# Kernel optimization log

Hardware: AMD Instinct MI355X
Metric: run time of the kernel (lower is better)

Reference implementation:

```python
import jax, jax.numpy as jnp
import numpy as np

HEADS = 8

def _ln(x, g, b):
    m = jnp.mean(x, -1, keepdims=True)
    v = jnp.var(x, -1, keepdims=True)
    return (x - m) * jax.lax.rsqrt(v + 1e-5) * g + b

def _mha(q, kv, W, b, key_valid):
    # W: [4,E,E] (q,k,v,out proj), b: [4,E]; key_valid: [Sk] bool mask over kv positions
    B, Sq, E = q.shape
    Sk = kv.shape[1]
    D = E // HEADS
    qh = (q @ W[0] + b[0]).reshape(B, Sq, HEADS, D)
    kh = (kv @ W[1] + b[1]).reshape(B, Sk, HEADS, D)
    vh = (kv @ W[2] + b[2]).reshape(B, Sk, HEADS, D)
    s = jnp.einsum('bqhd,bkhd->bhqk', qh, kh) / jnp.sqrt(jnp.asarray(D, q.dtype))
    s = jnp.where(key_valid[None, None, None, :], s, jnp.asarray(-1e9, q.dtype))
    o = jnp.einsum('bhqk,bkhd->bqhd', jax.nn.softmax(s, -1), vh).reshape(B, Sq, E)
    return o @ W[3] + b[3]

def _posenc(S, E):
    pos = np.arange(S)[:, None].astype(np.float32)
    i = np.arange(0, E, 2).astype(np.float32)[None, :]
    ang = pos / np.power(10000.0, i / E)
    pe = np.zeros((S, E), np.float32)
    pe[:, 0::2] = np.sin(ang)
    pe[:, 1::2] = np.cos(ang)
    return jnp.asarray(pe)

def _forward(noise, seeds, inemb_W, inemb_b, g_attn_W, g_attn_b, g_cross_W, g_cross_b,
             g_ffn_W1, g_ffn_b1, g_ffn_W2, g_ffn_b2, g_ln_g, g_ln_b,
             o_attn_W, o_attn_b, o_ffn_W1, o_ffn_b1, o_ffn_W2, o_ffn_b2, o_ln_g, o_ln_b,
             w2v, soft_W, soft_b):
    B, S, E = noise.shape
    V = soft_W.shape[1]
    # inEmb: M stacked linear layers (no activation)
    w = noise
    for i in range(inemb_W.shape[0]):
        w = w @ inemb_W[i] + inemb_b[i]
    pe = _posenc(S, E)[None]  # [1,S,E]
    nB = g_attn_W.shape[0]
    nO = o_attn_W.shape[0]

    def step(carry, t):
        Ybuf, out_sent = carry
        valid = jnp.arange(S) <= t  # grown-sequence mask (no KV cache in original)
        x = Ybuf + pe
        for i in range(nB):  # generator: outTrans decoder blocks (self + cross-attn to w)
            x = _ln(x + _mha(x, x, g_attn_W[i], g_attn_b[i], valid), g_ln_g[i, 0], g_ln_b[i, 0])
            x = _ln(x + _mha(x, w, g_cross_W[i], g_cross_b[i], valid), g_ln_g[i, 1], g_ln_b[i, 1])
            f = jax.nn.relu(x @ g_ffn_W1[i] + g_ffn_b1[i]) @ g_ffn_W2[i] + g_ffn_b2[i]
            x = _ln(x + f, g_ln_g[i, 2], g_ln_b[i, 2])
        for j in range(nO):  # outEmb: inTrans encoder blocks
            x = _ln(x + _mha(x, x, o_attn_W[j], o_attn_b[j], valid), o_ln_g[j, 0], o_ln_b[j, 0])
            f = jax.nn.relu(x @ o_ffn_W1[j] + o_ffn_b1[j]) @ o_ffn_W2[j] + o_ffn_b2[j]
            x = _ln(x + f, o_ln_g[j, 1], o_ln_b[j, 1])
        tok = x[:, t]  # [B,E]
        probs = jax.nn.softmax(tok @ soft_W + soft_b, axis=-1)  # [B,V]
        out_sent = jax.lax.dynamic_update_slice(out_sent, probs[:, None, :], (0, t, 0))
        emb = w2v[jnp.argmax(probs, axis=-1)]  # Word2Vec(one_hot(argmax)) == row lookup
        Ybuf = jax.lax.dynamic_update_slice(Ybuf, emb[:, None, :], (0, t, 0))
        return (Ybuf, out_sent), None

    init = (seeds, jnp.zeros((B, S, V), noise.dtype))
    (_, out_sent), _ = jax.lax.scan(step, init, jnp.arange(S))
    return out_sent

def setup_inputs():
    key = jax.random.key(0)
    ks = jax.random.split(key, 12)
    B, S, E, H, V = 32, 32, 512, 2048, 30000
    M, NB, NO = 2, 2, 1
    def rn(k, shape, s=0.02):
        return jax.random.normal(k, shape, jnp.float32) * s
    return {
        'noise': jax.random.normal(ks[0], (B, S, E), jnp.float32),
        'seeds': jax.random.normal(ks[1], (B, S, E), jnp.float32),
        'inemb_W': rn(ks[2], (M, E, E)), 'inemb_b': jnp.zeros((M, E), jnp.float32),
        'g_attn_W': rn(ks[3], (NB, 4, E, E)), 'g_attn_b': jnp.zeros((NB, 4, E), jnp.float32),
        'g_cross_W': rn(ks[4], (NB, 4, E, E)), 'g_cross_b': jnp.zeros((NB, 4, E), jnp.float32),
        'g_ffn_W1': rn(ks[5], (NB, E, H)), 'g_ffn_b1': jnp.zeros((NB, H), jnp.float32),
        'g_ffn_W2': rn(ks[6], (NB, H, E)), 'g_ffn_b2': jnp.zeros((NB, E), jnp.float32),
        'g_ln_g': jnp.ones((NB, 3, E), jnp.float32), 'g_ln_b': jnp.zeros((NB, 3, E), jnp.float32),
        'o_attn_W': rn(ks[7], (NO, 4, E, E)), 'o_attn_b': jnp.zeros((NO, 4, E), jnp.float32),
        'o_ffn_W1': rn(ks[8], (NO, E, H)), 'o_ffn_b1': jnp.zeros((NO, H), jnp.float32),
        'o_ffn_W2': rn(ks[9], (NO, H, E)), 'o_ffn_b2': jnp.zeros((NO, E), jnp.float32),
        'o_ln_g': jnp.ones((NO, 2, E), jnp.float32), 'o_ln_b': jnp.zeros((NO, 2, E), jnp.float32),
        'w2v': rn(ks[10], (V, E)),
        'soft_W': rn(ks[11], (E, V)), 'soft_b': jnp.zeros((V,), jnp.float32),
    }

def reference(noise, seeds, inemb_W, inemb_b, g_attn_W, g_attn_b, g_cross_W, g_cross_b,
              g_ffn_W1, g_ffn_b1, g_ffn_W2, g_ffn_b2, g_ln_g, g_ln_b,
              o_attn_W, o_attn_b, o_ffn_W1, o_ffn_b1, o_ffn_W2, o_ffn_b2, o_ln_g, o_ln_b,
              w2v, soft_W, soft_b):
    return _forward(noise, seeds, inemb_W, inemb_b, g_attn_W, g_attn_b, g_cross_W, g_cross_b,
                    g_ffn_W1, g_ffn_b1, g_ffn_W2, g_ffn_b2, g_ln_g, g_ln_b,
                    o_attn_W, o_attn_b, o_ffn_W1, o_ffn_b1, o_ffn_W2, o_ffn_b2, o_ln_g, o_ln_b,
                    w2v, soft_W, soft_b)
```

## Files before the change

### kernel.cpp

```cpp
#include <hip/hip_runtime.h>
#include <math.h>

#define E 512
#define S_MAX 32
#define BATCH 32
#define HEADS 8
#define DH 64
#define HID 2048
#define VOCAB 30000

__global__ void pe_kernel(float* __restrict__ PEp) {
    int s = blockIdx.x;
    for (int e = threadIdx.x; e < E; e += 256) {
        float expo = (float)(e & ~1) / (float)E;
        float den = powf(10000.0f, expo);
        float ang = (float)s / den;
        PEp[s * E + e] = (e & 1) ? cosf(ang) : sinf(ang);
    }
}

__global__ void build_x_kernel(float* __restrict__ X, const float* __restrict__ Ybuf,
                               const float* __restrict__ PEp, int Seff) {
    long idx = (long)blockIdx.x * 256 + threadIdx.x;
    long total = (long)BATCH * Seff * E;
    if (idx >= total) return;
    int e = (int)(idx & (E - 1));
    long m = idx >> 9;
    int b = (int)(m / Seff);
    int s = (int)(m - (long)b * Seff);
    X[idx] = Ybuf[((long)b * S_MAX + s) * E + e] + PEp[s * E + e];
}

template <int RELU>
__global__ __launch_bounds__(256) void gemm_kernel(const float* __restrict__ A,
                                                   const float* __restrict__ W,
                                                   const float* __restrict__ bias,
                                                   float* __restrict__ C,
                                                   int M, int N, int K,
                                                   long wz, long cz, long bz) {
    int z = blockIdx.z;
    W += (long)z * wz;
    C += (long)z * cz;
    bias += (long)z * bz;
    int n0 = blockIdx.x * 64;
    int m0 = blockIdx.y * 64;
    int tid = threadIdx.x;
    int tx = tid & 15, ty = tid >> 4;

    __shared__ float As[16][68];
    __shared__ float Ws[16][64];

    float acc[4][4];
#pragma unroll
    for (int i = 0; i < 4; i++)
#pragma unroll
        for (int j = 0; j < 4; j++) acc[i][j] = 0.f;

    for (int k0 = 0; k0 < K; k0 += 16) {
#pragma unroll
        for (int l = 0; l < 4; l++) {
            int idx = tid + l * 256;
            int m = idx >> 4, k = idx & 15;
            int mm = m0 + m;
            if (mm >= M) mm = M - 1;
            As[k][m] = A[(long)mm * K + k0 + k];
        }
#pragma unroll
        for (int l = 0; l < 4; l++) {
            int idx = tid + l * 256;
            int k = idx >> 6, n = idx & 63;
            Ws[k][n] = W[(long)(k0 + k) * N + n0 + n];
        }
        __syncthreads();
#pragma unroll
        for (int k = 0; k < 16; k++) {
            float a0 = As[k][ty * 4 + 0], a1 = As[k][ty * 4 + 1];
            float a2 = As[k][ty * 4 + 2], a3 = As[k][ty * 4 + 3];
            float w0 = Ws[k][tx * 4 + 0], w1 = Ws[k][tx * 4 + 1];
            float w2 = Ws[k][tx * 4 + 2], w3 = Ws[k][tx * 4 + 3];
            acc[0][0] += a0 * w0; acc[0][1] += a0 * w1; acc[0][2] += a0 * w2; acc[0][3] += a0 * w3;
            acc[1][0] += a1 * w0; acc[1][1] += a1 * w1; acc[1][2] += a1 * w2; acc[1][3] += a1 * w3;
            acc[2][0] += a2 * w0; acc[2][1] += a2 * w1; acc[2][2] += a2 * w2; acc[2][3] += a2 * w3;
            acc[3][0] += a3 * w0; acc[3][1] += a3 * w1; acc[3][2] += a3 * w2; acc[3][3] += a3 * w3;
        }
        __syncthreads();
    }
#pragma unroll
    for (int i = 0; i < 4; i++) {
        int m = m0 + ty * 4 + i;
        if (m < M) {
#pragma unroll
            for (int j = 0; j < 4; j++) {
                int n = n0 + tx * 4 + j;
                float v = acc[i][j] + bias[n];
                if (RELU) v = fmaxf(v, 0.f);
                C[(long)m * N + n] = v;
            }
        }
    }
}

__global__ __launch_bounds__(64) void attn_kernel(const float* __restrict__ Q,
                                                  const float* __restrict__ Kp,
                                                  const float* __restrict__ Vp,
                                                  float* __restrict__ O,
                                                  int Seff, int kvBatchStride) {
    int s = blockIdx.x, h = blockIdx.y, b = blockIdx.z;
    int lane = threadIdx.x;
    __shared__ float qs[DH];
    qs[lane] = Q[((long)(b * Seff + s)) * E + h * DH + lane];
    __syncthreads();

    float sc = -INFINITY;
    if (lane < Seff) {
        const float4* k4 = (const float4*)(Kp + (long)b * kvBatchStride + (long)lane * E + h * DH);
        const float4* q4 = (const float4*)qs;
        float acc = 0.f;
#pragma unroll
        for (int d = 0; d < DH / 4; d++) {
            float4 kv = k4[d];
            float4 qv = q4[d];
            acc += qv.x * kv.x;
            acc += qv.y * kv.y;
            acc += qv.z * kv.z;
            acc += qv.w * kv.w;
        }
        sc = acc * 0.125f;
    }
    float m = sc;
#pragma unroll
    for (int off = 32; off; off >>= 1) m = fmaxf(m, __shfl_xor(m, off));
    float p = (lane < Seff) ? expf(sc - m) : 0.f;
    float sum = p;
#pragma unroll
    for (int off = 32; off; off >>= 1) sum += __shfl_xor(sum, off);
    p = p / sum;

    float acc = 0.f;
    const float* vbase = Vp + (long)b * kvBatchStride + h * DH + lane;
    for (int k = 0; k < Seff; k++) {
        float pk = __shfl(p, k);
        acc = fmaf(pk, vbase[(long)k * E], acc);
    }
    O[((long)(b * Seff + s)) * E + h * DH + lane] = acc;
}

__global__ __launch_bounds__(64) void resid_ln_kernel(float* __restrict__ X,
                                                      const float* __restrict__ Dlt,
                                                      const float* __restrict__ g,
                                                      const float* __restrict__ bb) {
    long row = blockIdx.x;
    int lane = threadIdx.x;
    float* xr = X + row * E;
    const float* dr = Dlt + row * E;
    float v[8];
    float s = 0.f;
#pragma unroll
    for (int i = 0; i < 8; i++) {
        int e = lane + i * 64;
        v[i] = xr[e] + dr[e];
        s += v[i];
    }
#pragma unroll
    for (int off = 32; off; off >>= 1) s += __shfl_xor(s, off);
    float mean = s * (1.0f / E);
    float sq = 0.f;
#pragma unroll
    for (int i = 0; i < 8; i++) {
        float d = v[i] - mean;
        sq += d * d;
    }
#pragma unroll
    for (int off = 32; off; off >>= 1) sq += __shfl_xor(sq, off);
    float var = sq * (1.0f / E);
    float r = 1.0f / sqrtf(var + 1e-5f);
#pragma unroll
    for (int i = 0; i < 8; i++) {
        int e = lane + i * 64;
        xr[e] = (v[i] - mean) * r * g[e] + bb[e];
    }
}

__global__ __launch_bounds__(256) void logits_kernel(const float* __restrict__ X,
                                                     const float* __restrict__ SW,
                                                     const float* __restrict__ sb,
                                                     float* __restrict__ Lg,
                                                     int Seff, int t) {
    int nl = threadIdx.x & 63;
    int kq = threadIdx.x >> 6;
    int n = blockIdx.x * 64 + nl;
    bool nok = n < VOCAB;
    float acc[BATCH];
#pragma unroll
    for (int b = 0; b < BATCH; b++) acc[b] = 0.f;
    if (nok) {
        int k0 = kq * 128;
        for (int k = k0; k < k0 + 128; k++) {
            float wv = SW[(long)k * VOCAB + n];
#pragma unroll
            for (int b = 0; b < BATCH; b++) {
                acc[b] = fmaf(X[((long)(b * Seff + t)) * E + k], wv, acc[b]);
            }
        }
    }
    __shared__ float red[4][64];
    for (int b = 0; b < BATCH; b++) {
        red[kq][nl] = acc[b];
        __syncthreads();
        if (kq == 0 && nok) {
            float sum = red[0][nl] + red[1][nl] + red[2][nl] + red[3][nl] + sb[n];
            Lg[(long)b * VOCAB + n] = sum;
        }
        __syncthreads();
    }
}

__global__ __launch_bounds__(256) void softmax_out_kernel(const float* __restrict__ Lg,
                                                          float* __restrict__ Out,
                                                          const float* __restrict__ w2v,
                                                          float* __restrict__ Ybuf, int t) {
    int b = blockIdx.x;
    int tid = threadIdx.x;
    const float* lb = Lg + (long)b * VOCAB;
    __shared__ float red[256];

    float m = -INFINITY;
    for (int n = tid; n < VOCAB; n += 256) m = fmaxf(m, lb[n]);
    red[tid] = m;
    __syncthreads();
    for (int off = 128; off; off >>= 1) {
        if (tid < off) red[tid] = fmaxf(red[tid], red[tid + off]);
        __syncthreads();
    }
    m = red[0];
    __syncthreads();

    float s = 0.f;
    for (int n = tid; n < VOCAB; n += 256) s += expf(lb[n] - m);
    red[tid] = s;
    __syncthreads();
    for (int off = 128; off; off >>= 1) {
        if (tid < off) red[tid] += red[tid + off];
        __syncthreads();
    }
    s = red[0];
    __syncthreads();

    float bestv = -1.0f;
    int besti = VOCAB;
    float* ob = Out + ((long)b * S_MAX + t) * VOCAB;
    for (int n = tid; n < VOCAB; n += 256) {
        float p = expf(lb[n] - m) / s;
        ob[n] = p;
        if (p > bestv) { bestv = p; besti = n; }
    }
    __shared__ float rv[256];
    __shared__ int ri[256];
    rv[tid] = bestv;
    ri[tid] = besti;
    __syncthreads();
    for (int off = 128; off; off >>= 1) {
        if (tid < off) {
            float v2 = rv[tid + off];
            int i2 = ri[tid + off];
            if (v2 > rv[tid] || (v2 == rv[tid] && i2 < ri[tid])) { rv[tid] = v2; ri[tid] = i2; }
        }
        __syncthreads();
    }
    int idx = ri[0];
    float* yb = Ybuf + ((long)b * S_MAX + t) * E;
    for (int e = tid; e < E; e += 256) yb[e] = w2v[(long)idx * E + e];
}

extern "C" void kernel_launch(void* const* d_in, const int* in_sizes, int n_in,
                              void* d_out, int out_size, void* d_ws, size_t ws_size,
                              hipStream_t stream) {
    const float* noise    = (const float*)d_in[0];
    const float* seeds    = (const float*)d_in[1];
    const float* inemb_W  = (const float*)d_in[2];
    const float* inemb_b  = (const float*)d_in[3];
    const float* g_attn_W = (const float*)d_in[4];
    const float* g_attn_b = (const float*)d_in[5];
    const float* g_cross_W= (const float*)d_in[6];
    const float* g_cross_b= (const float*)d_in[7];
    const float* g_ffn_W1 = (const float*)d_in[8];
    const float* g_ffn_b1 = (const float*)d_in[9];
    const float* g_ffn_W2 = (const float*)d_in[10];
    const float* g_ffn_b2 = (const float*)d_in[11];
    const float* g_ln_g   = (const float*)d_in[12];
    const float* g_ln_b   = (const float*)d_in[13];
    const float* o_attn_W = (const float*)d_in[14];
    const float* o_attn_b = (const float*)d_in[15];
    const float* o_ffn_W1 = (const float*)d_in[16];
    const float* o_ffn_b1 = (const float*)d_in[17];
    const float* o_ffn_W2 = (const float*)d_in[18];
    const float* o_ffn_b2 = (const float*)d_in[19];
    const float* o_ln_g   = (const float*)d_in[20];
    const float* o_ln_b   = (const float*)d_in[21];
    const float* w2v      = (const float*)d_in[22];
    const float* soft_W   = (const float*)d_in[23];
    const float* soft_b   = (const float*)d_in[24];
    float* out = (float*)d_out;
    float* ws = (float*)d_ws;

    const long EE  = (long)E * E;
    const long BSE = (long)BATCH * S_MAX * E;

    float* PE   = ws;
    float* WEMB = PE + 16384;
    float* KWVW = WEMB + BSE;
    float* YBUF = KWVW + 4 * BSE;
    float* X    = YBUF + BSE;
    float* QKV  = X + BSE;
    float* AOUT = QKV + 3 * BSE;
    float* TMP  = AOUT + BSE;
    float* HB   = TMP + BSE;
    float* LG   = HB + (long)BATCH * S_MAX * HID;

    auto GEMM = [&](const float* A, const float* W, const float* bias, float* C,
                    int M, int N, int K, int Z, long wz, long cz, long bz, bool relu) {
        dim3 g(N / 64, (M + 63) / 64, Z);
        if (relu)
            gemm_kernel<1><<<g, dim3(256), 0, stream>>>(A, W, bias, C, M, N, K, wz, cz, bz);
        else
            gemm_kernel<0><<<g, dim3(256), 0, stream>>>(A, W, bias, C, M, N, K, wz, cz, bz);
    };

    pe_kernel<<<dim3(S_MAX), dim3(256), 0, stream>>>(PE);
    hipMemcpyAsync(YBUF, seeds, BSE * sizeof(float), hipMemcpyDeviceToDevice, stream);

    GEMM(noise, inemb_W, inemb_b, QKV, BATCH * S_MAX, E, E, 1, 0, 0, 0, false);
    GEMM(QKV, inemb_W + EE, inemb_b + E, WEMB, BATCH * S_MAX, E, E, 1, 0, 0, 0, false);

    for (int i = 0; i < 2; i++) {
        GEMM(WEMB, g_cross_W + i * 4 * EE + EE, g_cross_b + i * 4 * E + E,
             KWVW + i * 2 * BSE, BATCH * S_MAX, E, E, 2, EE, BSE, E, false);
    }

    for (int t = 0; t < S_MAX; t++) {
        int Seff = t + 1;
        int Mrows = BATCH * Seff;
        long ME = (long)Mrows * E;
        int total = Mrows * E;

        build_x_kernel<<<dim3((total + 255) / 256), dim3(256), 0, stream>>>(X, YBUF, PE, Seff);

        for (int i = 0; i < 2; i++) {
            const float* AW = g_attn_W + i * 4 * EE;
            const float* Ab = g_attn_b + i * 4 * E;
            GEMM(X, AW, Ab, QKV, Mrows, E, E, 3, EE, ME, E, false);
            attn_kernel<<<dim3(Seff, HEADS, BATCH), dim3(64), 0, stream>>>(
                QKV, QKV + ME, QKV + 2 * ME, AOUT, Seff, Seff * E);
            GEMM(AOUT, AW + 3 * EE, Ab + 3 * E, TMP, Mrows, E, E, 1, 0, 0, 0, false);
            resid_ln_kernel<<<dim3(Mrows), dim3(64), 0, stream>>>(
                X, TMP, g_ln_g + (i * 3 + 0) * E, g_ln_b + (i * 3 + 0) * E);
            const float* CW = g_cross_W + i * 4 * EE;
            const float* Cb = g_cross_b + i * 4 * E;
            GEMM(X, CW, Cb, QKV, Mrows, E, E, 1, 0, 0, 0, false);
            attn_kernel<<<dim3(Seff, HEADS, BATCH), dim3(64), 0, stream>>>(
                QKV, KWVW + i * 2 * BSE, KWVW + i * 2 * BSE + BSE, AOUT, Seff, S_MAX * E);
            GEMM(AOUT, CW + 3 * EE, Cb + 3 * E, TMP, Mrows, E, E, 1, 0, 0, 0, false);
            resid_ln_kernel<<<dim3(Mrows), dim3(64), 0, stream>>>(
                X, TMP, g_ln_g + (i * 3 + 1) * E, g_ln_b + (i * 3 + 1) * E);
            GEMM(X, g_ffn_W1 + i * (long)E * HID, g_ffn_b1 + i * HID, HB, Mrows, HID, E,
                 1, 0, 0, 0, true);
            GEMM(HB, g_ffn_W2 + i * (long)HID * E, g_ffn_b2 + i * E, TMP, Mrows, E, HID,
                 1, 0, 0, 0, false);
            resid_ln_kernel<<<dim3(Mrows), dim3(64), 0, stream>>>(
                X, TMP, g_ln_g + (i * 3 + 2) * E, g_ln_b + (i * 3 + 2) * E);
        }
        GEMM(X, o_attn_W, o_attn_b, QKV, Mrows, E, E, 3, EE, ME, E, false);
        attn_kernel<<<dim3(Seff, HEADS, BATCH), dim3(64), 0, stream>>>(
            QKV, QKV + ME, QKV + 2 * ME, AOUT, Seff, Seff * E);
        GEMM(AOUT, o_attn_W + 3 * EE, o_attn_b + 3 * E, TMP, Mrows, E, E, 1, 0, 0, 0, false);
        resid_ln_kernel<<<dim3(Mrows), dim3(64), 0, stream>>>(X, TMP, o_ln_g, o_ln_b);
        GEMM(X, o_ffn_W1, o_ffn_b1, HB, Mrows, HID, E, 1, 0, 0, 0, true);
        GEMM(HB, o_ffn_W2, o_ffn_b2, TMP, Mrows, E, HID, 1, 0, 0, 0, false);
        resid_ln_kernel<<<dim3(Mrows), dim3(64), 0, stream>>>(X, TMP, o_ln_g + E, o_ln_b + E);

        logits_kernel<<<dim3((VOCAB + 63) / 64), dim3(256), 0, stream>>>(X, soft_W, soft_b, LG, Seff, t);
        softmax_out_kernel<<<dim3(BATCH), dim3(256), 0, stream>>>(LG, out, w2v, YBUF, t);
    }
}
```

Baseline: 32.73 ms.

## Replace FP32 SIMT GEMMs with three-way bf16-split MFMA GEMMs

Replaces the scalar FP32 tiled GEMM with an MFMA bf16 GEMM. To keep near-FP32 accuracy, each operand is split into high, mid and low bf16 parts and six cross-product MFMAs are accumulated. Weights are pre-split and transposed once per call when workspace allows, otherwise per GEMM. Producer kernels (build_x, attention, layernorm, GEMM epilogues) now emit split activations directly. This trades six MFMA passes and extra split storage and traffic for matrix-core throughput in place of FP32 FMA loops.

```diff
diff --git a/kernel.cpp b/kernel.cpp
--- a/kernel.cpp
+++ b/kernel.cpp
@@ -9,6 +9,26 @@
 #define HID 2048
 #define VOCAB 30000
 
+typedef unsigned short u16;
+typedef __attribute__((ext_vector_type(8))) short short8;
+typedef __attribute__((ext_vector_type(4))) float f32x4;
+
+__device__ __forceinline__ u16 f2bf(float x) {
+    union { float f; unsigned u; } v; v.f = x;
+    unsigned r = v.u + 0x7fffu + ((v.u >> 16) & 1u);
+    return (u16)(r >> 16);
+}
+__device__ __forceinline__ float bf2f(u16 h) {
+    union { unsigned u; float f; } v; v.u = ((unsigned)h) << 16;
+    return v.f;
+}
+__device__ __forceinline__ void split3(float x, u16& h, u16& m, u16& l) {
+    h = f2bf(x); float hf = bf2f(h);
+    float r1 = x - hf;
+    m = f2bf(r1); float mf = bf2f(m);
+    l = f2bf(r1 - mf);
+}
+
 __global__ void pe_kernel(float* __restrict__ PEp) {
     int s = blockIdx.x;
     for (int e = threadIdx.x; e < E; e += 256) {
@@ -20,81 +40,155 @@
 }
 
 __global__ void build_x_kernel(float* __restrict__ X, const float* __restrict__ Ybuf,
-                               const float* __restrict__ PEp, int Seff) {
+                               const float* __restrict__ PEp, int Seff,
+                               u16* __restrict__ Xh, u16* __restrict__ Xm, u16* __restrict__ Xl) {
     long idx = (long)blockIdx.x * 256 + threadIdx.x;
     long total = (long)BATCH * Seff * E;
     if (idx >= total) return;
     int e = (int)(idx & (E - 1));
-    long m = idx >> 9;
-    int b = (int)(m / Seff);
-    int s = (int)(m - (long)b * Seff);
-    X[idx] = Ybuf[((long)b * S_MAX + s) * E + e] + PEp[s * E + e];
-}
-
-template <int RELU>
-__global__ __launch_bounds__(256) void gemm_kernel(const float* __restrict__ A,
-                                                   const float* __restrict__ W,
-                                                   const float* __restrict__ bias,
-                                                   float* __restrict__ C,
-                                                   int M, int N, int K,
-                                                   long wz, long cz, long bz) {
+    long mm = idx >> 9;
+    int b = (int)(mm / Seff);
+    int s = (int)(mm - (long)b * Seff);
+    float v = Ybuf[((long)b * S_MAX + s) * E + e] + PEp[s * E + e];
+    X[idx] = v;
+    u16 h, m, l; split3(v, h, m, l);
+    Xh[idx] = h; Xm[idx] = m; Xl[idx] = l;
+}
+
+__global__ void split_act_kernel(const float* __restrict__ in, long n,
+                                 u16* __restrict__ Ph, u16* __restrict__ Pm, u16* __restrict__ Pl) {
+    long i = ((long)blockIdx.x * 256 + threadIdx.x) * 4;
+    if (i >= n) return;
+    float4 v = *(const float4*)(in + i);
+    u16 h, m, l;
+    split3(v.x, h, m, l); Ph[i] = h; Pm[i] = m; Pl[i] = l;
+    split3(v.y, h, m, l); Ph[i+1] = h; Pm[i+1] = m; Pl[i+1] = l;
+    split3(v.z, h, m, l); Ph[i+2] = h; Pm[i+2] = m; Pl[i+2] = l;
+    split3(v.w, h, m, l); Ph[i+3] = h; Pm[i+3] = m; Pl[i+3] = l;
+}
+
+__global__ __launch_bounds__(256) void wsplit_kernel(const float* __restrict__ W,
+                                                     u16* __restrict__ Ph, u16* __restrict__ Pm,
+                                                     u16* __restrict__ Pl,
+                                                     int K, int N, long wzin, long wzout) {
     int z = blockIdx.z;
-    W += (long)z * wz;
+    W += (long)z * wzin; Ph += (long)z * wzout; Pm += (long)z * wzout; Pl += (long)z * wzout;
+    int n0 = blockIdx.x * 32, k0 = blockIdx.y * 32;
+    __shared__ float T[32][33];
+    int tid = threadIdx.x;
+    int kk = tid >> 3, nn = (tid & 7) * 4;
+    float4 v = *(const float4*)&W[(long)(k0 + kk) * N + n0 + nn];
+    T[kk][nn + 0] = v.x; T[kk][nn + 1] = v.y; T[kk][nn + 2] = v.z; T[kk][nn + 3] = v.w;
+    __syncthreads();
+    int n = tid >> 3, k4 = (tid & 7) * 4;
+    u16 h[4], m[4], l[4];
+#pragma unroll
+    for (int j = 0; j < 4; j++) split3(T[k4 + j][n], h[j], m[j], l[j]);
+    long o = (long)(n0 + n) * K + k0 + k4;
+    *(ushort4*)&Ph[o] = make_ushort4(h[0], h[1], h[2], h[3]);
+    *(ushort4*)&Pm[o] = make_ushort4(m[0], m[1], m[2], m[3]);
+    *(ushort4*)&Pl[o] = make_ushort4(l[0], l[1], l[2], l[3]);
+}
+
+template <int RELU, int WF32, int WSPLIT>
+__global__ __launch_bounds__(256) void gemm_mfma(
+    const u16* __restrict__ Ah, const u16* __restrict__ Am, const u16* __restrict__ Al,
+    const u16* __restrict__ Wh, const u16* __restrict__ Wm, const u16* __restrict__ Wl,
+    const float* __restrict__ bias,
+    float* __restrict__ C, u16* __restrict__ Ch, u16* __restrict__ Cm, u16* __restrict__ Cl,
+    int M, int N, int K, long wz, long cz, long bz) {
+    int z = blockIdx.z;
+    const u16* Ap[3] = {Ah, Am, Al};
+    const u16* Bp[3] = {Wh + (long)z * wz, Wm + (long)z * wz, Wl + (long)z * wz};
+    bias += (long)z * bz;
     C += (long)z * cz;
-    bias += (long)z * bz;
-    int n0 = blockIdx.x * 64;
-    int m0 = blockIdx.y * 64;
-    int tid = threadIdx.x;
-    int tx = tid & 15, ty = tid >> 4;
-
-    __shared__ float As[16][68];
-    __shared__ float Ws[16][64];
-
-    float acc[4][4];
-#pragma unroll
-    for (int i = 0; i < 4; i++)
-#pragma unroll
-        for (int j = 0; j < 4; j++) acc[i][j] = 0.f;
-
-    for (int k0 = 0; k0 < K; k0 += 16) {
-#pragma unroll
-        for (int l = 0; l < 4; l++) {
-            int idx = tid + l * 256;
-            int m = idx >> 4, k = idx & 15;
-            int mm = m0 + m;
-            if (mm >= M) mm = M - 1;
-            As[k][m] = A[(long)mm * K + k0 + k];
-        }
-#pragma unroll
-        for (int l = 0; l < 4; l++) {
-            int idx = tid + l * 256;
-            int k = idx >> 6, n = idx & 63;
-            Ws[k][n] = W[(long)(k0 + k) * N + n0 + n];
-        }
-        __syncthreads();
-#pragma unroll
-        for (int k = 0; k < 16; k++) {
-            float a0 = As[k][ty * 4 + 0], a1 = As[k][ty * 4 + 1];
-            float a2 = As[k][ty * 4 + 2], a3 = As[k][ty * 4 + 3];
-            float w0 = Ws[k][tx * 4 + 0], w1 = Ws[k][tx * 4 + 1];
-            float w2 = Ws[k][tx * 4 + 2], w3 = Ws[k][tx * 4 + 3];
-            acc[0][0] += a0 * w0; acc[0][1] += a0 * w1; acc[0][2] += a0 * w2; acc[0][3] += a0 * w3;
-            acc[1][0] += a1 * w0; acc[1][1] += a1 * w1; acc[1][2] += a1 * w2; acc[1][3] += a1 * w3;
-            acc[2][0] += a2 * w0; acc[2][1] += a2 * w1; acc[2][2] += a2 * w2; acc[2][3] += a2 * w3;
-            acc[3][0] += a3 * w0; acc[3][1] += a3 * w1; acc[3][2] += a3 * w2; acc[3][3] += a3 * w3;
-        }
-        __syncthreads();
-    }
-#pragma unroll
-    for (int i = 0; i < 4; i++) {
-        int m = m0 + ty * 4 + i;
-        if (m < M) {
+    Ch += (long)z * cz; Cm += (long)z * cz; Cl += (long)z * cz;
+
+    int n0 = blockIdx.x * 64, m0 = blockIdx.y * 64;
+    int tid = threadIdx.x, lane = tid & 63, wid = tid >> 6;
+    int wr = wid >> 1, wc = wid & 1;
+
+    __shared__ u16 As[3][2048];
+    __shared__ u16 Bs[3][2048];
+
+    int srow = (tid >> 6) * 16 + (tid & 15);
+    int scol = ((tid >> 4) & 3) * 8;
+    int arow = m0 + srow; if (arow >= M) arow = M - 1;
+    int brow = n0 + srow;
+    long abase = (long)arow * K + scol;
+    long bbase = (long)brow * K + scol;
+
+    uint4 ra[3], rb[3];
+#pragma unroll
+    for (int p = 0; p < 3; p++) {
+        ra[p] = *(const uint4*)(Ap[p] + abase);
+        rb[p] = *(const uint4*)(Bp[p] + bbase);
+    }
+
+    f32x4 acc[2][2];
+#pragma unroll
+    for (int mi = 0; mi < 2; mi++)
+#pragma unroll
+        for (int ni = 0; ni < 2; ni++) acc[mi][ni] = (f32x4){0.f, 0.f, 0.f, 0.f};
+
+    int fro = (lane >> 4) * 128 + (lane & 15) * 8;
+    const int PA[6] = {0, 0, 1, 1, 0, 2};
+    const int PB[6] = {0, 1, 0, 1, 2, 0};
+
+    for (int k0 = 0; k0 < K; k0 += 32) {
+#pragma unroll
+        for (int p = 0; p < 3; p++) {
+            *(uint4*)&As[p][tid * 8] = ra[p];
+            *(uint4*)&Bs[p][tid * 8] = rb[p];
+        }
+        __syncthreads();
+        if (k0 + 32 < K) {
+#pragma unroll
+            for (int p = 0; p < 3; p++) {
+                ra[p] = *(const uint4*)(Ap[p] + abase + k0 + 32);
+                rb[p] = *(const uint4*)(Bp[p] + bbase + k0 + 32);
+            }
+        }
+        short8 af[3][2], bf[3][2];
+#pragma unroll
+        for (int p = 0; p < 3; p++) {
+#pragma unroll
+            for (int q = 0; q < 2; q++) {
+                af[p][q] = *(const short8*)&As[p][(wr * 2 + q) * 512 + fro];
+                bf[p][q] = *(const short8*)&Bs[p][(wc * 2 + q) * 512 + fro];
+            }
+        }
+#pragma unroll
+        for (int u = 0; u < 6; u++) {
+#pragma unroll
+            for (int mi = 0; mi < 2; mi++)
+#pragma unroll
+                for (int ni = 0; ni < 2; ni++)
+                    acc[mi][ni] = __builtin_amdgcn_mfma_f32_16x16x32_bf16(
+                        af[PA[u]][mi], bf[PB[u]][ni], acc[mi][ni], 0, 0, 0);
+        }
+        __syncthreads();
+    }
+
+#pragma unroll
+    for (int mi = 0; mi < 2; mi++) {
+#pragma unroll
+        for (int ni = 0; ni < 2; ni++) {
+            int col = n0 + wc * 32 + ni * 16 + (lane & 15);
+            float bv = bias[col];
 #pragma unroll
             for (int j = 0; j < 4; j++) {
-                int n = n0 + tx * 4 + j;
-                float v = acc[i][j] + bias[n];
-                if (RELU) v = fmaxf(v, 0.f);
-                C[(long)m * N + n] = v;
+                int row = m0 + wr * 32 + mi * 16 + (lane >> 4) * 4 + j;
+                if (row < M) {
+                    float v = acc[mi][ni][j] + bv;
+                    if (RELU) v = fmaxf(v, 0.f);
+                    long idx = (long)row * N + col;
+                    if (WF32) C[idx] = v;
+                    if (WSPLIT) {
+                        u16 hh, mm, ll; split3(v, hh, mm, ll);
+                        Ch[idx] = hh; Cm[idx] = mm; Cl[idx] = ll;
+                    }
+                }
             }
         }
     }
@@ -103,7 +197,8 @@
 __global__ __launch_bounds__(64) void attn_kernel(const float* __restrict__ Q,
                                                   const float* __restrict__ Kp,
                                                   const float* __restrict__ Vp,
-                                                  float* __restrict__ O,
+                                                  u16* __restrict__ Oh, u16* __restrict__ Om,
+                                                  u16* __restrict__ Ol,
                                                   int Seff, int kvBatchStride) {
     int s = blockIdx.x, h = blockIdx.y, b = blockIdx.z;
     int lane = threadIdx.x;
@@ -120,10 +215,7 @@
         for (int d = 0; d < DH / 4; d++) {
             float4 kv = k4[d];
             float4 qv = q4[d];
-            acc += qv.x * kv.x;
-            acc += qv.y * kv.y;
-            acc += qv.z * kv.z;
-            acc += qv.w * kv.w;
+            acc += qv.x * kv.x; acc += qv.y * kv.y; acc += qv.z * kv.z; acc += qv.w * kv.w;
         }
         sc = acc * 0.125f;
     }
@@ -142,13 +234,17 @@
         float pk = __shfl(p, k);
         acc = fmaf(pk, vbase[(long)k * E], acc);
     }
-    O[((long)(b * Seff + s)) * E + h * DH + lane] = acc;
+    long o = ((long)(b * Seff + s)) * E + h * DH + lane;
+    u16 hh, mm, ll; split3(acc, hh, mm, ll);
+    Oh[o] = hh; Om[o] = mm; Ol[o] = ll;
 }
 
 __global__ __launch_bounds__(64) void resid_ln_kernel(float* __restrict__ X,
                                                       const float* __restrict__ Dlt,
                                                       const float* __restrict__ g,
-                                                      const float* __restrict__ bb) {
+                                                      const float* __restrict__ bb,
+                                                      u16* __restrict__ Xh, u16* __restrict__ Xm,
+                                                      u16* __restrict__ Xl) {
     long row = blockIdx.x;
     int lane = threadIdx.x;
     float* xr = X + row * E;
@@ -177,7 +273,11 @@
 #pragma unroll
     for (int i = 0; i < 8; i++) {
         int e = lane + i * 64;
-        xr[e] = (v[i] - mean) * r * g[e] + bb[e];
+        float o = (v[i] - mean) * r * g[e] + bb[e];
+        xr[e] = o;
+        u16 hh, mm, ll; split3(o, hh, mm, ll);
+        long idx = row * E + e;
+        Xh[idx] = hh; Xm[idx] = mm; Xl[idx] = ll;
     }
 }
 
@@ -304,37 +404,91 @@
     float* ws = (float*)d_ws;
 
     const long EE  = (long)E * E;
+    const long EH  = (long)E * HID;
     const long BSE = (long)BATCH * S_MAX * E;
-
-    float* PE   = ws;
-    float* WEMB = PE + 16384;
-    float* KWVW = WEMB + BSE;
-    float* YBUF = KWVW + 4 * BSE;
-    float* X    = YBUF + BSE;
-    float* QKV  = X + BSE;
-    float* AOUT = QKV + 3 * BSE;
-    float* TMP  = AOUT + BSE;
-    float* HB   = TMP + BSE;
-    float* LG   = HB + (long)BATCH * S_MAX * HID;
-
-    auto GEMM = [&](const float* A, const float* W, const float* bias, float* C,
-                    int M, int N, int K, int Z, long wz, long cz, long bz, bool relu) {
+    const long BSH = (long)BATCH * S_MAX * HID;
+    const long WTOT = 46 * EE;
+
+    long off = 0;
+    float* PE   = ws + off; off += 16384;
+    float* YBUF = ws + off; off += BSE;
+    float* X    = ws + off; off += BSE;
+    float* TMP  = ws + off; off += BSE;
+    float* QKV  = ws + off; off += 3 * BSE;
+    float* KWVW = ws + off; off += 4 * BSE;
+    float* LG   = ws + off; off += 960000;
+    u16* XsH = (u16*)(ws + off); off += 3 * BSE / 2;
+    u16* XsM = XsH + BSE; u16* XsL = XsM + BSE;
+    u16* AOH = (u16*)(ws + off); off += 3 * BSE / 2;
+    u16* AOM = AOH + BSE; u16* AOL = AOM + BSE;
+    u16* HBH = (u16*)(ws + off); off += 3 * BSH / 2;
+    u16* HBM2 = HBH + BSH; u16* HBL = HBM2 + BSH;
+    long baseWords = off;
+
+    bool full = ws_size >= (size_t)(baseWords + 3 * WTOT / 2) * 4;
+    long WT_ELEMS = full ? WTOT : 4 * EE;
+    u16* WT_H = (u16*)(ws + baseWords);
+    u16* WT_M = WT_H + WT_ELEMS;
+    u16* WT_L = WT_M + WT_ELEMS;
+
+    const long OFF_INEMB = 0;
+    const long OFF_GATTN = 2 * EE;
+    const long OFF_GCROSS = 10 * EE;
+    const long OFF_OATTN = 18 * EE;
+    const long OFF_GF1 = 22 * EE;
+    const long OFF_GF2 = 30 * EE;
+    const long OFF_OF1 = 38 * EE;
+    const long OFF_OF2 = 42 * EE;
+
+    auto WSPL = [&](const float* Wsrc, long offFull, int K, int N, int z) -> long {
+        if (full) return offFull;
+        wsplit_kernel<<<dim3(N / 32, K / 32, z), dim3(256), 0, stream>>>(
+            Wsrc, WT_H, WT_M, WT_L, K, N, (long)K * N, (long)K * N);
+        return 0;
+    };
+
+    auto GEMM = [&](const u16* Ah, const u16* Am, const u16* Al, long woff,
+                    const float* bias, float* C, u16* Ch, u16* Cm, u16* Cl,
+                    int M, int N, int K, int Z, long wz, long cz, long bz, int mode) {
         dim3 g(N / 64, (M + 63) / 64, Z);
-        if (relu)
-            gemm_kernel<1><<<g, dim3(256), 0, stream>>>(A, W, bias, C, M, N, K, wz, cz, bz);
+        const u16* Wh = WT_H + woff; const u16* Wm = WT_M + woff; const u16* Wl = WT_L + woff;
+        if (mode == 0)
+            gemm_mfma<0, 1, 0><<<g, dim3(256), 0, stream>>>(Ah, Am, Al, Wh, Wm, Wl, bias,
+                                                            C, Ch, Cm, Cl, M, N, K, wz, cz, bz);
+        else if (mode == 1)
+            gemm_mfma<0, 0, 1><<<g, dim3(256), 0, stream>>>(Ah, Am, Al, Wh, Wm, Wl, bias,
+                                                            C, Ch, Cm, Cl, M, N, K, wz, cz, bz);
         else
-            gemm_kernel<0><<<g, dim3(256), 0, stream>>>(A, W, bias, C, M, N, K, wz, cz, bz);
+            gemm_mfma<1, 0, 1><<<g, dim3(256), 0, stream>>>(Ah, Am, Al, Wh, Wm, Wl, bias,
+                                                            C, Ch, Cm, Cl, M, N, K, wz, cz, bz);
     };
 
     pe_kernel<<<dim3(S_MAX), dim3(256), 0, stream>>>(PE);
     hipMemcpyAsync(YBUF, seeds, BSE * sizeof(float), hipMemcpyDeviceToDevice, stream);
 
-    GEMM(noise, inemb_W, inemb_b, QKV, BATCH * S_MAX, E, E, 1, 0, 0, 0, false);
-    GEMM(QKV, inemb_W + EE, inemb_b + E, WEMB, BATCH * S_MAX, E, E, 1, 0, 0, 0, false);
-
+    if (full) {
+        wsplit_kernel<<<dim3(16, 16, 2), dim3(256), 0, stream>>>(inemb_W, WT_H + OFF_INEMB, WT_M + OFF_INEMB, WT_L + OFF_INEMB, 512, 512, EE, EE);
+        wsplit_kernel<<<dim3(16, 16, 8), dim3(256), 0, stream>>>(g_attn_W, WT_H + OFF_GATTN, WT_M + OFF_GATTN, WT_L + OFF_GATTN, 512, 512, EE, EE);
+        wsplit_kernel<<<dim3(16, 16, 8), dim3(256), 0, stream>>>(g_cross_W, WT_H + OFF_GCROSS, WT_M + OFF_GCROSS, WT_L + OFF_GCROSS, 512, 512, EE, EE);
+        wsplit_kernel<<<dim3(16, 16, 4), dim3(256), 0, stream>>>(o_attn_W, WT_H + OFF_OATTN, WT_M + OFF_OATTN, WT_L + OFF_OATTN, 512, 512, EE, EE);
+        wsplit_kernel<<<dim3(64, 16, 2), dim3(256), 0, stream>>>(g_ffn_W1, WT_H + OFF_GF1, WT_M + OFF_GF1, WT_L + OFF_GF1, 512, 2048, EH, EH);
+        wsplit_kernel<<<dim3(16, 64, 2), dim3(256), 0, stream>>>(g_ffn_W2, WT_H + OFF_GF2, WT_M + OFF_GF2, WT_L + OFF_GF2, 2048, 512, EH, EH);
+        wsplit_kernel<<<dim3(64, 16, 1), dim3(256), 0, stream>>>(o_ffn_W1, WT_H + OFF_OF1, WT_M + OFF_OF1, WT_L + OFF_OF1, 512, 2048, EH, EH);
+        wsplit_kernel<<<dim3(16, 64, 1), dim3(256), 0, stream>>>(o_ffn_W2, WT_H + OFF_OF2, WT_M + OFF_OF2, WT_L + OFF_OF2, 2048, 512, EH, EH);
+    }
+
+    split_act_kernel<<<dim3((int)(BSE / 1024)), dim3(256), 0, stream>>>(noise, BSE, HBH, HBM2, HBL);
+
+    {
+        long w = WSPL(inemb_W, OFF_INEMB, 512, 512, 1);
+        GEMM(HBH, HBM2, HBL, w, inemb_b, TMP, AOH, AOM, AOL, BATCH * S_MAX, E, E, 1, 0, 0, 0, 1);
+        w = WSPL(inemb_W + EE, OFF_INEMB + EE, 512, 512, 1);
+        GEMM(AOH, AOM, AOL, w, inemb_b + E, TMP, XsH, XsM, XsL, BATCH * S_MAX, E, E, 1, 0, 0, 0, 1);
+    }
     for (int i = 0; i < 2; i++) {
-        GEMM(WEMB, g_cross_W + i * 4 * EE + EE, g_cross_b + i * 4 * E + E,
-             KWVW + i * 2 * BSE, BATCH * S_MAX, E, E, 2, EE, BSE, E, false);
+        long w = WSPL(g_cross_W + (i * 4 + 1) * EE, OFF_GCROSS + (i * 4 + 1) * EE, 512, 512, 2);
+        GEMM(XsH, XsM, XsL, w, g_cross_b + (i * 4 + 1) * E, KWVW + i * 2 * BSE, AOH, AOM, AOL,
+             BATCH * S_MAX, E, E, 2, EE, BSE, E, 0);
     }
 
     for (int t = 0; t < S_MAX; t++) {
@@ -343,40 +497,55 @@
         long ME = (long)Mrows * E;
         int total = Mrows * E;
 
-        build_x_kernel<<<dim3((total + 255) / 256), dim3(256), 0, stream>>>(X, YBUF, PE, Seff);
+        build_x_kernel<<<dim3((total + 255) / 256), dim3(256), 0, stream>>>(X, YBUF, PE, Seff,
+                                                                            XsH, XsM, XsL);
 
         for (int i = 0; i < 2; i++) {
-            const float* AW = g_attn_W + i * 4 * EE;
-            const float* Ab = g_attn_b + i * 4 * E;
-            GEMM(X, AW, Ab, QKV, Mrows, E, E, 3, EE, ME, E, false);
+            long w = WSPL(g_attn_W + (long)i * 4 * EE, OFF_GATTN + i * 4 * EE, 512, 512, 3);
+            GEMM(XsH, XsM, XsL, w, g_attn_b + (long)i * 4 * E, QKV, AOH, AOM, AOL,
+                 Mrows, E, E, 3, EE, ME, E, 0);
             attn_kernel<<<dim3(Seff, HEADS, BATCH), dim3(64), 0, stream>>>(
-                QKV, QKV + ME, QKV + 2 * ME, AOUT, Seff, Seff * E);
-            GEMM(AOUT, AW + 3 * EE, Ab + 3 * E, TMP, Mrows, E, E, 1, 0, 0, 0, false);
+                QKV, QKV + ME, QKV + 2 * ME, AOH, AOM, AOL, Seff, Seff * E);
+            w = WSPL(g_attn_W + (i * 4 + 3) * EE, OFF_GATTN + (i * 4 + 3) * EE, 512, 512, 1);
+            GEMM(AOH, AOM, AOL, w, g_attn_b + (i * 4 + 3) * E, TMP, AOH, AOM, AOL,
+                 Mrows, E, E, 1, 0, 0, 0, 0);
             resid_ln_kernel<<<dim3(Mrows), dim3(64), 0, stream>>>(
-                X, TMP, g_ln_g + (i * 3 + 0) * E, g_ln_b + (i * 3 + 0) * E);
-            const float* CW = g_cross_W + i * 4 * EE;
-            const float* Cb = g_cross_b + i * 4 * E;
-            GEMM(X, CW, Cb, QKV, Mrows, E, E, 1, 0, 0, 0, false);
+                X, TMP, g_ln_g + (i * 3 + 0) * E, g_ln_b + (i * 3 + 0) * E, XsH, XsM, XsL);
+            w = WSPL(g_cross_W + (long)i * 4 * EE, OFF_GCROSS + i * 4 * EE, 512, 512, 1);
+            GEMM(XsH, XsM, XsL, w, g_cross_b + (long)i * 4 * E, QKV, AOH, AOM, AOL,
+                 Mrows, E, E, 1, 0, 0, 0, 0);
             attn_kernel<<<dim3(Seff, HEADS, BATCH), dim3(64), 0, stream>>>(
-                QKV, KWVW + i * 2 * BSE, KWVW + i * 2 * BSE + BSE, AOUT, Seff, S_MAX * E);
-            GEMM(AOUT, CW + 3 * EE, Cb + 3 * E, TMP, Mrows, E, E, 1, 0, 0, 0, false);
+                QKV, KWVW + i * 2 * BSE, KWVW + i * 2 * BSE + BSE, AOH, AOM, AOL, Seff, S_MAX * E);
+            w = WSPL(g_cross_W + (i * 4 + 3) * EE, OFF_GCROSS + (i * 4 + 3) * EE, 512, 512, 1);
+            GEMM(AOH, AOM, AOL, w, g_cross_b + (i * 4 + 3) * E, TMP, AOH, AOM, AOL,
+                 Mrows, E, E, 1, 0, 0, 0, 0);
             resid_ln_kernel<<<dim3(Mrows), dim3(64), 0, stream>>>(
-                X, TMP, g_ln_g + (i * 3 + 1) * E, g_ln_b + (i * 3 + 1) * E);
-            GEMM(X, g_ffn_W1 + i * (long)E * HID, g_ffn_b1 + i * HID, HB, Mrows, HID, E,
-                 1, 0, 0, 0, true);
-            GEMM(HB, g_ffn_W2 + i * (long)HID * E, g_ffn_b2 + i * E, TMP, Mrows, E, HID,
-                 1, 0, 0, 0, false);
+                X, TMP, g_ln_g + (i * 3 + 1) * E, g_ln_b + (i * 3 + 1) * E, XsH, XsM, XsL);
+            w = WSPL(g_ffn_W1 + (long)i * EH, OFF_GF1 + i * EH, 512, 2048, 1);
+            GEMM(XsH, XsM, XsL, w, g_ffn_b1 + (long)i * HID, TMP, HBH, HBM2, HBL,
+                 Mrows, HID, E, 1, 0, 0, 0, 2);
+            w = WSPL(g_ffn_W2 + (long)i * EH, OFF_GF2 + i * EH, 2048, 512, 1);
+            GEMM(HBH, HBM2, HBL, w, g_ffn_b2 + (long)i * E, TMP, AOH, AOM, AOL,
+                 Mrows, E, HID, 1, 0, 0, 0, 0);
             resid_ln_kernel<<<dim3(Mrows), dim3(64), 0, stream>>>(
-                X, TMP, g_ln_g + (i * 3 + 2) * E, g_ln_b + (i * 3 + 2) * E);
-        }
-        GEMM(X, o_attn_W, o_attn_b, QKV, Mrows, E, E, 3, EE, ME, E, false);
-        attn_kernel<<<dim3(Seff, HEADS, BATCH), dim3(64), 0, stream>>>(
-            QKV, QKV + ME, QKV + 2 * ME, AOUT, Seff, Seff * E);
-        GEMM(AOUT, o_attn_W + 3 * EE, o_attn_b + 3 * E, TMP, Mrows, E, E, 1, 0, 0, 0, false);
-        resid_ln_kernel<<<dim3(Mrows), dim3(64), 0, stream>>>(X, TMP, o_ln_g, o_ln_b);
-        GEMM(X, o_ffn_W1, o_ffn_b1, HB, Mrows, HID, E, 1, 0, 0, 0, true);
-        GEMM(HB, o_ffn_W2, o_ffn_b2, TMP, Mrows, E, HID, 1, 0, 0, 0, false);
-        resid_ln_kernel<<<dim3(Mrows), dim3(64), 0, stream>>>(X, TMP, o_ln_g + E, o_ln_b + E);
+                X, TMP, g_ln_g + (i * 3 + 2) * E, g_ln_b + (i * 3 + 2) * E, XsH, XsM, XsL);
+        }
+        {
+            long w = WSPL(o_attn_W, OFF_OATTN, 512, 512, 3);
+            GEMM(XsH, XsM, XsL, w, o_attn_b, QKV, AOH, AOM, AOL, Mrows, E, E, 3, EE, ME, E, 0);
+            attn_kernel<<<dim3(Seff, HEADS, BATCH), dim3(64), 0, stream>>>(
+                QKV, QKV + ME, QKV + 2 * ME, AOH, AOM, AOL, Seff, Seff * E);
+            w = WSPL(o_attn_W + 3 * EE, OFF_OATTN + 3 * EE, 512, 512, 1);
+            GEMM(AOH, AOM, AOL, w, o_attn_b + 3 * E, TMP, AOH, AOM, AOL, Mrows, E, E, 1, 0, 0, 0, 0);
+            resid_ln_kernel<<<dim3(Mrows), dim3(64), 0, stream>>>(X, TMP, o_ln_g, o_ln_b,
+                                                                  XsH, XsM, XsL);
+            w = WSPL(o_ffn_W1, OFF_OF1, 512, 2048, 1);
+            GEMM(XsH, XsM, XsL, w, o_ffn_b1, TMP, HBH, HBM2, HBL, Mrows, HID, E, 1, 0, 0, 0, 2);
+            w = WSPL(o_ffn_W2, OFF_OF2, 2048, 512, 1);
+            GEMM(HBH, HBM2, HBL, w, o_ffn_b2, TMP, AOH, AOM, AOL, Mrows, E, HID, 1, 0, 0, 0, 0);
+            resid_ln_kernel<<<dim3(Mrows), dim3(64), 0, stream>>>(X, TMP, o_ln_g + E, o_ln_b + E,
+                                                                  XsH, XsM, XsL);
+        }
 
         logits_kernel<<<dim3((VOCAB + 63) / 64), dim3(256), 0, stream>>>(X, soft_W, soft_b, LG, Seff, t);
         softmax_out_kernel<<<dim3(BATCH), dim3(256), 0, stream>>>(LG, out, w2v, YBUF, t);
```

Result: slower. 37.35 ms (+14.1%).
